# Kernel tuning notes

Hardware: AMD Instinct MI355X
Metric: run time of the kernel (lower is better)

## Reference

```python
import jax, jax.numpy as jnp
import numpy as np


def _sage_layer(x, neighbors, W, b):
    # x: (N, D), neighbors: (N, deg) int indices into x
    neigh_agg = x[neighbors].mean(axis=1)           # (N, D) gather + mean
    h = jnp.concatenate([x, neigh_agg], axis=-1)     # (N, 2D)
    return jax.nn.relu(h @ W + b)                    # (N, D_out)


def setup_inputs() -> dict:
    key = jax.random.key(0)
    k1, k2, k3, k4 = jax.random.split(key, 4)
    N, D, DEG = 50000, 128, 16
    x = jax.random.normal(k1, (N, D), dtype=jnp.float32)
    neighbors = jax.random.randint(k2, (N, DEG), 0, N)
    # Linear(in_dim*2, out_dim) weights, stored as (2D, D_out) for x @ W
    scale = 1.0 / np.sqrt(2 * D)
    W1 = jax.random.normal(k3, (2 * D, D), dtype=jnp.float32) * scale
    b1 = jnp.zeros((D,), dtype=jnp.float32)
    W2 = jax.random.normal(k4, (2 * D, D), dtype=jnp.float32) * scale
    b2 = jnp.zeros((D,), dtype=jnp.float32)
    return {"x": x, "neighbors": neighbors, "W1": W1, "b1": b1, "W2": W2, "b2": b2}


def reference(x, neighbors, W1, b1, W2, b2):
    h = _sage_layer(x, neighbors, W1, b1)
    h = _sage_layer(h, neighbors, W2, b2)
    return h
```

## Files before the change

kernel.cpp:

```cpp
#include <hip/hip_runtime.h>

typedef __attribute__((ext_vector_type(8))) short short8;
typedef __attribute__((ext_vector_type(4))) float f32x4;
typedef __attribute__((ext_vector_type(2))) float f32x2;

#define N_NODES 50000
#define D 128
#define DEG 16
#define K2 256
#define BM 32

static __device__ __forceinline__ unsigned short f2b(float f) {
    union { float f; unsigned int u; } v; v.f = f;
    return (unsigned short)((v.u + 0x7fffu + ((v.u >> 16) & 1u)) >> 16);
}

__global__ void prep(const float* __restrict__ x, unsigned short* __restrict__ xb,
                     const float* __restrict__ W1, const float* __restrict__ W2,
                     unsigned short* __restrict__ Wf1, unsigned short* __restrict__ Wf2) {
    int b = blockIdx.x;
    if (b < 32) {
        int o  = (b * 256 + threadIdx.x) * 4;
        int e0 = o & 7;
        int l  = (o >> 3) & 63;
        int ct = (o >> 9) & 1;
        int kk = (o >> 10) & 7;
        int w  = o >> 13;
        int n  = w * 32 + ct * 16 + (l & 15);
        int kb = kk * 32 + (l >> 4) * 8 + e0;
        ushort4 a, c;
        a.x = f2b(W1[(kb + 0) * D + n]);
        a.y = f2b(W1[(kb + 1) * D + n]);
        a.z = f2b(W1[(kb + 2) * D + n]);
        a.w = f2b(W1[(kb + 3) * D + n]);
        *(ushort4*)(Wf1 + o) = a;
        c.x = f2b(W2[(kb + 0) * D + n]);
        c.y = f2b(W2[(kb + 1) * D + n]);
        c.z = f2b(W2[(kb + 2) * D + n]);
        c.w = f2b(W2[(kb + 3) * D + n]);
        *(ushort4*)(Wf2 + o) = c;
    } else {
        int i = ((b - 32) * 256 + threadIdx.x) * 4;
        if (i < N_NODES * D) {
            float4 v = *(const float4*)(x + i);
            ushort4 o4;
            o4.x = f2b(v.x); o4.y = f2b(v.y); o4.z = f2b(v.z); o4.w = f2b(v.w);
            *(ushort4*)(xb + i) = o4;
        }
    }
}

template <int OUT_BF16>
__global__ __launch_bounds__(256, 4)
void sage_layer(const unsigned short* __restrict__ feat,
                const int* __restrict__ nbr,
                const unsigned short* __restrict__ wf,
                const float* __restrict__ bias,
                void* __restrict__ out)
{
    __shared__ __align__(16) unsigned short Hl[BM * 264];
    __shared__ int Nl[BM * DEG];
    const int tid  = threadIdx.x;
    const int row0 = blockIdx.x * BM;

    if (tid < 128) {
        int g = row0 * DEG + tid * 4;
        int gmax = N_NODES * DEG - 4;
        if (g > gmax) g = gmax;
        *(int4*)(Nl + tid * 4) = *(const int4*)(nbr + g);
    }
    __syncthreads();

    const char* fb = (const char*)feat;

    #pragma unroll
    for (int p = 0; p < 2; ++p) {
        int a = tid + p * 256;
        int r = a >> 4;
        int s = a & 15;
        int grow = row0 + r;
        if (grow >= N_NODES) grow = N_NODES - 1;
        unsigned sB = (unsigned)s * 16u;
        short8 self = *(const short8*)(fb + (unsigned)grow * 256u + sB);

        int4 i0 = *(const int4*)(Nl + r * 16);
        int4 i1 = *(const int4*)(Nl + r * 16 + 4);
        int4 i2 = *(const int4*)(Nl + r * 16 + 8);
        int4 i3 = *(const int4*)(Nl + r * 16 + 12);
        int ids[16] = { i0.x, i0.y, i0.z, i0.w, i1.x, i1.y, i1.z, i1.w,
                        i2.x, i2.y, i2.z, i2.w, i3.x, i3.y, i3.z, i3.w };

        short8 v[16];
        #pragma unroll
        for (int j = 0; j < 16; ++j)
            v[j] = *(const short8*)(fb + (((unsigned)ids[j]) << 8) + sB);

        f32x2 am[4];
        #pragma unroll
        for (int i = 0; i < 4; ++i) am[i] = (f32x2){0.f, 0.f};
        #pragma unroll
        for (int j = 0; j < 16; ++j) {
            union { short8 s8; unsigned u[4]; } vv; vv.s8 = v[j];
            #pragma unroll
            for (int i = 0; i < 4; ++i) {
                unsigned ui = vv.u[i];
                f32x2 e;
                e.x = __uint_as_float(ui << 16);
                e.y = __uint_as_float(ui & 0xffff0000u);
                am[i] += e;
            }
        }

        unsigned short* hr = Hl + r * 264 + s * 8;
        *(short8*)(hr) = self;
        union { unsigned short u[8]; short8 s8; } m;
        #pragma unroll
        for (int i = 0; i < 4; ++i) {
            m.u[2 * i]     = f2b(am[i].x * 0.0625f);
            m.u[2 * i + 1] = f2b(am[i].y * 0.0625f);
        }
        *(short8*)(hr + D) = m.s8;
    }

    const int lane = tid & 63;
    const int w    = tid >> 6;
    const int quad = lane >> 4;
    const int l16  = lane & 15;
    const int n_base = w * 32;
    const unsigned short* wfw = wf + w * 8192;
    short8 bfrag[8][2];
    #pragma unroll
    for (int kk = 0; kk < 8; ++kk)
        #pragma unroll
        for (int ct = 0; ct < 2; ++ct)
            bfrag[kk][ct] = *(const short8*)(wfw + kk * 1024 + ct * 512 + lane * 8);

    __syncthreads();

    f32x4 acc[2][2];
    #pragma unroll
    for (int rt = 0; rt < 2; ++rt)
        #pragma unroll
        for (int ct = 0; ct < 2; ++ct)
            acc[rt][ct] = (f32x4){0.f, 0.f, 0.f, 0.f};

    #pragma unroll
    for (int kk = 0; kk < 8; ++kk) {
        short8 afrag[2];
        #pragma unroll
        for (int rt = 0; rt < 2; ++rt)
            afrag[rt] = *(const short8*)(&Hl[(rt * 16 + l16) * 264 + kk * 32 + quad * 8]);
        #pragma unroll
        for (int rt = 0; rt < 2; ++rt)
            #pragma unroll
            for (int ct = 0; ct < 2; ++ct)
                acc[rt][ct] = __builtin_amdgcn_mfma_f32_16x16x32_bf16(
                    afrag[rt], bfrag[kk][ct], acc[rt][ct], 0, 0, 0);
    }

    float bv0 = bias[n_base + l16];
    float bv1 = bias[n_base + 16 + l16];
    #pragma unroll
    for (int rt = 0; rt < 2; ++rt) {
        int grow_base = row0 + rt * 16 + quad * 4;
        #pragma unroll
        for (int r = 0; r < 4; ++r) {
            int grow = grow_base + r;
            if (grow >= N_NODES) continue;
            #pragma unroll
            for (int ct = 0; ct < 2; ++ct) {
                float vv = acc[rt][ct][r] + (ct ? bv1 : bv0);
                vv = vv > 0.f ? vv : 0.f;
                int col = n_base + ct * 16 + l16;
                if (OUT_BF16)
                    ((unsigned short*)out)[grow * D + col] = f2b(vv);
                else
                    ((float*)out)[grow * D + col] = vv;
            }
        }
    }
}

extern "C" void kernel_launch(void* const* d_in, const int* in_sizes, int n_in,
                              void* d_out, int out_size, void* d_ws, size_t ws_size,
                              hipStream_t stream) {
    const float* x  = (const float*)d_in[0];
    const int*   nb = (const int*)d_in[1];
    const float* W1 = (const float*)d_in[2];
    const float* b1 = (const float*)d_in[3];
    const float* W2 = (const float*)d_in[4];
    const float* b2 = (const float*)d_in[5];

    char* ws = (char*)d_ws;
    unsigned short* Wf1 = (unsigned short*)(ws);
    unsigned short* Wf2 = (unsigned short*)(ws + 65536);
    unsigned short* xb  = (unsigned short*)(ws + 131072);
    unsigned short* h1  = (unsigned short*)(ws + 131072 + 12800000);

    prep<<<32 + 6250, 256, 0, stream>>>(x, xb, W1, W2, Wf1, Wf2);

    const int mgrid = (N_NODES + BM - 1) / BM;
    sage_layer<1><<<mgrid, 256, 0, stream>>>(xb, nb, Wf1, b1, h1);
    sage_layer<0><<<mgrid, 256, 0, stream>>>(h1, nb, Wf2, b2, d_out);
}
```

Baseline: 144.1 us.

## Reorder GraphSAGE as transform-then-aggregate with split self/neighbor GEMM

Uses linearity of the mean to compute P = x·W_self and Z = x·W_neigh first in a dense GEMM kernel, then gathers and averages rows of Z per node and adds P, bias and ReLU in a separate aggregation kernel. The GEMM tile is staged into shared memory via global_load_lds with an XOR swizzle, and the weight prep is re-laid out to produce both halves as a single 256-column fragment set. This turns the fused gather+GEMM into two simpler passes, at the cost of writing and rereading intermediate P (fp32) and Z (bf16) buffers and doubling the kernel launches. Z is rounded to bf16 before averaging, which slightly changes numerics.

Result: slower. 167.5 us (+16.2%).

```diff
diff --git a/kernel.cpp b/kernel.cpp
--- a/kernel.cpp
+++ b/kernel.cpp
@@ -7,8 +7,6 @@
 #define N_NODES 50000
 #define D 128
 #define DEG 16
-#define K2 256
-#define BM 32
 
 static __device__ __forceinline__ unsigned short f2b(float f) {
     union { float f; unsigned int u; } v; v.f = f;
@@ -20,25 +18,26 @@
                      unsigned short* __restrict__ Wf1, unsigned short* __restrict__ Wf2) {
     int b = blockIdx.x;
     if (b < 32) {
-        int o  = (b * 256 + threadIdx.x) * 4;
-        int e0 = o & 7;
-        int l  = (o >> 3) & 63;
-        int ct = (o >> 9) & 1;
-        int kk = (o >> 10) & 7;
-        int w  = o >> 13;
-        int n  = w * 32 + ct * 16 + (l & 15);
-        int kb = kk * 32 + (l >> 4) * 8 + e0;
-        ushort4 a, c;
-        a.x = f2b(W1[(kb + 0) * D + n]);
-        a.y = f2b(W1[(kb + 1) * D + n]);
-        a.z = f2b(W1[(kb + 2) * D + n]);
-        a.w = f2b(W1[(kb + 3) * D + n]);
+        int idx = b * 256 + threadIdx.x;
+        int o   = idx * 4;
+        int e0  = o & 7;
+        int l   = (o >> 3) & 63;
+        int ct2 = (o >> 9) & 1;
+        int kk  = (o >> 10) & 3;
+        int w2  = (o >> 12) & 7;
+        int c   = w2 * 32 + ((l & 15) << 1) + ct2;
+        int kin = kk * 32 + (l >> 4) * 8 + e0;
+        int krow = (c < 128) ? kin : 128 + kin;
+        int ccol = c & 127;
+        const float* s1 = W1 + krow * D + ccol;
+        const float* s2 = W2 + krow * D + ccol;
+        ushort4 a, cc;
+        a.x  = f2b(s1[0]);     a.y  = f2b(s1[D]);
+        a.z  = f2b(s1[2 * D]); a.w  = f2b(s1[3 * D]);
         *(ushort4*)(Wf1 + o) = a;
-        c.x = f2b(W2[(kb + 0) * D + n]);
-        c.y = f2b(W2[(kb + 1) * D + n]);
-        c.z = f2b(W2[(kb + 2) * D + n]);
-        c.w = f2b(W2[(kb + 3) * D + n]);
-        *(ushort4*)(Wf2 + o) = c;
+        cc.x = f2b(s2[0]);     cc.y = f2b(s2[D]);
+        cc.z = f2b(s2[2 * D]); cc.w = f2b(s2[3 * D]);
+        *(ushort4*)(Wf2 + o) = cc;
     } else {
         int i = ((b - 32) * 256 + threadIdx.x) * 4;
         if (i < N_NODES * D) {
@@ -50,134 +49,170 @@
     }
 }
 
+__global__ __launch_bounds__(256, 4)
+void gemm_pz(const unsigned short* __restrict__ feat,
+             const unsigned short* __restrict__ wf,
+             float* __restrict__ P,
+             unsigned short* __restrict__ Z)
+{
+    __shared__ __align__(16) unsigned short Al[32 * 128];
+    const int tid  = threadIdx.x;
+    const int row0 = blockIdx.x * 32;
+    const int wave = tid >> 6;
+    const int lane = tid & 63;
+    const int quad = lane >> 4;
+    const int l16  = lane & 15;
+
+    #pragma unroll
+    for (int i = 0; i < 2; ++i) {
+        unsigned o    = (unsigned)tid * 16u + (unsigned)i * 4096u;
+        unsigned row  = o >> 8;
+        unsigned colb = o & 255u;
+        unsigned scol = colb ^ ((row & 7u) << 4);
+        int grow = row0 + (int)row;
+        if (grow >= N_NODES) grow = N_NODES - 1;
+        const char* src = (const char*)feat + (unsigned)grow * 256u + scol;
+        __builtin_amdgcn_global_load_lds(
+            (const __attribute__((address_space(1))) unsigned int*)src,
+            (__attribute__((address_space(3))) unsigned int*)
+                ((char*)Al + wave * 1024 + i * 4096),
+            16, 0, 0);
+    }
+
+    short8 bfrag[4][4];
+    #pragma unroll
+    for (int kk = 0; kk < 4; ++kk)
+        #pragma unroll
+        for (int ct = 0; ct < 4; ++ct) {
+            int w2 = 2 * wave + (ct >> 1), ct2 = ct & 1;
+            bfrag[kk][ct] = *(const short8*)(wf + w2 * 4096 + kk * 1024 + ct2 * 512 + lane * 8);
+        }
+
+    __syncthreads();
+
+    f32x4 acc[2][4];
+    #pragma unroll
+    for (int rt = 0; rt < 2; ++rt)
+        #pragma unroll
+        for (int ct = 0; ct < 4; ++ct)
+            acc[rt][ct] = (f32x4){0.f, 0.f, 0.f, 0.f};
+
+    #pragma unroll
+    for (int kk = 0; kk < 4; ++kk) {
+        short8 af[2];
+        #pragma unroll
+        for (int rt = 0; rt < 2; ++rt) {
+            unsigned row  = (unsigned)(rt * 16 + l16);
+            unsigned byte = row * 256u + (unsigned)kk * 64u + (unsigned)quad * 16u;
+            byte ^= (row & 7u) << 4;
+            af[rt] = *(const short8*)((const char*)Al + byte);
+        }
+        #pragma unroll
+        for (int rt = 0; rt < 2; ++rt)
+            #pragma unroll
+            for (int ct = 0; ct < 4; ++ct)
+                acc[rt][ct] = __builtin_amdgcn_mfma_f32_16x16x32_bf16(
+                    af[rt], bfrag[kk][ct], acc[rt][ct], 0, 0, 0);
+    }
+
+    #pragma unroll
+    for (int ctp = 0; ctp < 2; ++ctp) {
+        int c0 = (2 * wave + ctp) * 32 + (l16 << 1);
+        #pragma unroll
+        for (int rt = 0; rt < 2; ++rt) {
+            int gb = row0 + rt * 16 + quad * 4;
+            #pragma unroll
+            for (int r = 0; r < 4; ++r) {
+                int grow = gb + r;
+                if (grow >= N_NODES) continue;
+                float v0 = acc[rt][2 * ctp][r];
+                float v1 = acc[rt][2 * ctp + 1][r];
+                if (c0 < 128) {
+                    f32x2 o2; o2.x = v0; o2.y = v1;
+                    *(f32x2*)(P + grow * D + c0) = o2;
+                } else {
+                    unsigned u = (unsigned)f2b(v0) | ((unsigned)f2b(v1) << 16);
+                    *(unsigned*)(Z + grow * D + (c0 - 128)) = u;
+                }
+            }
+        }
+    }
+}
+
 template <int OUT_BF16>
 __global__ __launch_bounds__(256, 4)
-void sage_layer(const unsigned short* __restrict__ feat,
-                const int* __restrict__ nbr,
-                const unsigned short* __restrict__ wf,
-                const float* __restrict__ bias,
-                void* __restrict__ out)
+void agg(const unsigned short* __restrict__ Z,
+         const float* __restrict__ P,
+         const int* __restrict__ nbr,
+         const float* __restrict__ bias,
+         void* __restrict__ out)
 {
-    __shared__ __align__(16) unsigned short Hl[BM * 264];
-    __shared__ int Nl[BM * DEG];
+    __shared__ __align__(16) int Nl[256];
     const int tid  = threadIdx.x;
-    const int row0 = blockIdx.x * BM;
-
-    if (tid < 128) {
-        int g = row0 * DEG + tid * 4;
-        int gmax = N_NODES * DEG - 4;
-        if (g > gmax) g = gmax;
-        *(int4*)(Nl + tid * 4) = *(const int4*)(nbr + g);
-    }
+    const int row0 = blockIdx.x << 4;
+    Nl[tid] = nbr[(row0 << 4) + tid];
     __syncthreads();
 
-    const char* fb = (const char*)feat;
-
-    #pragma unroll
-    for (int p = 0; p < 2; ++p) {
-        int a = tid + p * 256;
-        int r = a >> 4;
-        int s = a & 15;
-        int grow = row0 + r;
-        if (grow >= N_NODES) grow = N_NODES - 1;
-        unsigned sB = (unsigned)s * 16u;
-        short8 self = *(const short8*)(fb + (unsigned)grow * 256u + sB);
-
-        int4 i0 = *(const int4*)(Nl + r * 16);
-        int4 i1 = *(const int4*)(Nl + r * 16 + 4);
-        int4 i2 = *(const int4*)(Nl + r * 16 + 8);
-        int4 i3 = *(const int4*)(Nl + r * 16 + 12);
-        int ids[16] = { i0.x, i0.y, i0.z, i0.w, i1.x, i1.y, i1.z, i1.w,
-                        i2.x, i2.y, i2.z, i2.w, i3.x, i3.y, i3.z, i3.w };
-
-        short8 v[16];
-        #pragma unroll
-        for (int j = 0; j < 16; ++j)
-            v[j] = *(const short8*)(fb + (((unsigned)ids[j]) << 8) + sB);
-
-        f32x2 am[4];
-        #pragma unroll
-        for (int i = 0; i < 4; ++i) am[i] = (f32x2){0.f, 0.f};
-        #pragma unroll
-        for (int j = 0; j < 16; ++j) {
-            union { short8 s8; unsigned u[4]; } vv; vv.s8 = v[j];
-            #pragma unroll
-            for (int i = 0; i < 4; ++i) {
-                unsigned ui = vv.u[i];
-                f32x2 e;
-                e.x = __uint_as_float(ui << 16);
-                e.y = __uint_as_float(ui & 0xffff0000u);
-                am[i] += e;
-            }
-        }
-
-        unsigned short* hr = Hl + r * 264 + s * 8;
-        *(short8*)(hr) = self;
+    const int r = tid >> 4, s = tid & 15;
+    const int grow = row0 + r;
+    const char* zb = (const char*)Z;
+    const unsigned sB = (unsigned)s << 4;
+
+    int4 i0 = *(const int4*)(Nl + r * 16);
+    int4 i1 = *(const int4*)(Nl + r * 16 + 4);
+    int4 i2 = *(const int4*)(Nl + r * 16 + 8);
+    int4 i3 = *(const int4*)(Nl + r * 16 + 12);
+    int ids[16] = { i0.x, i0.y, i0.z, i0.w, i1.x, i1.y, i1.z, i1.w,
+                    i2.x, i2.y, i2.z, i2.w, i3.x, i3.y, i3.z, i3.w };
+
+    short8 v[16];
+    #pragma unroll
+    for (int j = 0; j < 16; ++j)
+        v[j] = *(const short8*)(zb + (((unsigned)ids[j]) << 8) + sB);
+
+    f32x2 am[4];
+    #pragma unroll
+    for (int i = 0; i < 4; ++i) am[i] = (f32x2){0.f, 0.f};
+    #pragma unroll
+    for (int j = 0; j < 16; ++j) {
+        union { short8 s8; unsigned u[4]; } vv; vv.s8 = v[j];
+        #pragma unroll
+        for (int i = 0; i < 4; ++i) {
+            unsigned ui = vv.u[i];
+            f32x2 e;
+            e.x = __uint_as_float(ui << 16);
+            e.y = __uint_as_float(ui & 0xffff0000u);
+            am[i] += e;
+        }
+    }
+
+    f32x4 p0 = *(const f32x4*)(P + grow * D + s * 8);
+    f32x4 p1 = *(const f32x4*)(P + grow * D + s * 8 + 4);
+    f32x4 b0 = *(const f32x4*)(bias + s * 8);
+    f32x4 b1 = *(const f32x4*)(bias + s * 8 + 4);
+
+    float o[8];
+    o[0] = p0.x + b0.x + am[0].x * 0.0625f;
+    o[1] = p0.y + b0.y + am[0].y * 0.0625f;
+    o[2] = p0.z + b0.z + am[1].x * 0.0625f;
+    o[3] = p0.w + b0.w + am[1].y * 0.0625f;
+    o[4] = p1.x + b1.x + am[2].x * 0.0625f;
+    o[5] = p1.y + b1.y + am[2].y * 0.0625f;
+    o[6] = p1.z + b1.z + am[3].x * 0.0625f;
+    o[7] = p1.w + b1.w + am[3].y * 0.0625f;
+    #pragma unroll
+    for (int i = 0; i < 8; ++i) o[i] = o[i] > 0.f ? o[i] : 0.f;
+
+    if (OUT_BF16) {
         union { unsigned short u[8]; short8 s8; } m;
         #pragma unroll
-        for (int i = 0; i < 4; ++i) {
-            m.u[2 * i]     = f2b(am[i].x * 0.0625f);
-            m.u[2 * i + 1] = f2b(am[i].y * 0.0625f);
-        }
-        *(short8*)(hr + D) = m.s8;
-    }
-
-    const int lane = tid & 63;
-    const int w    = tid >> 6;
-    const int quad = lane >> 4;
-    const int l16  = lane & 15;
-    const int n_base = w * 32;
-    const unsigned short* wfw = wf + w * 8192;
-    short8 bfrag[8][2];
-    #pragma unroll
-    for (int kk = 0; kk < 8; ++kk)
-        #pragma unroll
-        for (int ct = 0; ct < 2; ++ct)
-            bfrag[kk][ct] = *(const short8*)(wfw + kk * 1024 + ct * 512 + lane * 8);
-
-    __syncthreads();
-
-    f32x4 acc[2][2];
-    #pragma unroll
-    for (int rt = 0; rt < 2; ++rt)
-        #pragma unroll
-        for (int ct = 0; ct < 2; ++ct)
-            acc[rt][ct] = (f32x4){0.f, 0.f, 0.f, 0.f};
-
-    #pragma unroll
-    for (int kk = 0; kk < 8; ++kk) {
-        short8 afrag[2];
-        #pragma unroll
-        for (int rt = 0; rt < 2; ++rt)
-            afrag[rt] = *(const short8*)(&Hl[(rt * 16 + l16) * 264 + kk * 32 + quad * 8]);
-        #pragma unroll
-        for (int rt = 0; rt < 2; ++rt)
-            #pragma unroll
-            for (int ct = 0; ct < 2; ++ct)
-                acc[rt][ct] = __builtin_amdgcn_mfma_f32_16x16x32_bf16(
-                    afrag[rt], bfrag[kk][ct], acc[rt][ct], 0, 0, 0);
-    }
-
-    float bv0 = bias[n_base + l16];
-    float bv1 = bias[n_base + 16 + l16];
-    #pragma unroll
-    for (int rt = 0; rt < 2; ++rt) {
-        int grow_base = row0 + rt * 16 + quad * 4;
-        #pragma unroll
-        for (int r = 0; r < 4; ++r) {
-            int grow = grow_base + r;
-            if (grow >= N_NODES) continue;
-            #pragma unroll
-            for (int ct = 0; ct < 2; ++ct) {
-                float vv = acc[rt][ct][r] + (ct ? bv1 : bv0);
-                vv = vv > 0.f ? vv : 0.f;
-                int col = n_base + ct * 16 + l16;
-                if (OUT_BF16)
-                    ((unsigned short*)out)[grow * D + col] = f2b(vv);
-                else
-                    ((float*)out)[grow * D + col] = vv;
-            }
-        }
+        for (int i = 0; i < 8; ++i) m.u[i] = f2b(o[i]);
+        *(short8*)((unsigned short*)out + grow * D + s * 8) = m.s8;
+    } else {
+        f32x4 q0; q0.x = o[0]; q0.y = o[1]; q0.z = o[2]; q0.w = o[3];
+        f32x4 q1; q1.x = o[4]; q1.y = o[5]; q1.z = o[6]; q1.w = o[7];
+        *(f32x4*)((float*)out + grow * D + s * 8) = q0;
+        *(f32x4*)((float*)out + grow * D + s * 8 + 4) = q1;
     }
 }
 
@@ -196,10 +231,16 @@
     unsigned short* Wf2 = (unsigned short*)(ws + 65536);
     unsigned short* xb  = (unsigned short*)(ws + 131072);
     unsigned short* h1  = (unsigned short*)(ws + 131072 + 12800000);
+    unsigned short* Zb  = (unsigned short*)(ws + 131072 + 25600000);
+    float*          Pb  = (float*)(ws + 131072 + 38400000);
 
     prep<<<32 + 6250, 256, 0, stream>>>(x, xb, W1, W2, Wf1, Wf2);
 
-    const int mgrid = (N_NODES + BM - 1) / BM;
-    sage_layer<1><<<mgrid, 256, 0, stream>>>(xb, nb, Wf1, b1, h1);
-    sage_layer<0><<<mgrid, 256, 0, stream>>>(h1, nb, Wf2, b2, d_out);
-}
+    const int ggrid = (N_NODES + 31) / 32;
+    const int agrid = N_NODES / 16;
+
+    gemm_pz<<<ggrid, 256, 0, stream>>>(xb, Wf1, Pb, Zb);
+    agg<1><<<agrid, 256, 0, stream>>>(Zb, Pb, nb, b1, h1);
+    gemm_pz<<<ggrid, 256, 0, stream>>>(h1, Wf2, Pb, Zb);
+    agg<0><<<agrid, 256, 0, stream>>>(Zb, Pb, nb, b2, d_out);
+}
```
